# Kernel tuning notes

Measured on AMD Instinct MI355X. Metric: run time of the kernel, lower is better.

Reference implementation:

```python
import jax, jax.numpy as jnp
import numpy as np

D = 2048
N_HEADS = 16
N_KV = 4
HEAD_DIM = D // N_HEADS  # 128
N_REP = N_HEADS // N_KV  # 4
B, S = 2, 2048


def setup_inputs() -> dict:
    key = jax.random.key(0)
    ks = jax.random.split(key, 5)
    scale = 0.02
    return {
        "x": jax.random.normal(ks[0], (B, S, D), dtype=jnp.float32),
        "wq": jax.random.normal(ks[1], (D, N_HEADS * HEAD_DIM), dtype=jnp.float32) * scale,
        "wk": jax.random.normal(ks[2], (D, N_KV * HEAD_DIM), dtype=jnp.float32) * scale,
        "wv": jax.random.normal(ks[3], (D, N_KV * HEAD_DIM), dtype=jnp.float32) * scale,
        "wo": jax.random.normal(ks[4], (N_HEADS * HEAD_DIM, D), dtype=jnp.float32) * scale,
    }


def reference(x, wq, wk, wv, wo):
    b, s, _ = x.shape
    # projections
    xq = (x @ wq).reshape(b, s, N_HEADS, HEAD_DIM)
    xk = (x @ wk).reshape(b, s, N_KV, HEAD_DIM)
    xv = (x @ wv).reshape(b, s, N_KV, HEAD_DIM)
    # GQA: group queries per kv head -> [b, n_kv, n_rep, s, d]
    xq = xq.transpose(0, 2, 1, 3).reshape(b, N_KV, N_REP, s, HEAD_DIM)
    xk = xk.transpose(0, 2, 1, 3)  # [b, n_kv, s, d]
    xv = xv.transpose(0, 2, 1, 3)
    scale = 1.0 / jnp.sqrt(jnp.asarray(HEAD_DIM, dtype=x.dtype))
    scores = jnp.einsum('bkrqd,bkvd->bkrqv', xq, xk) * scale  # [b,n_kv,n_rep,s,s]
    causal = jnp.triu(jnp.ones((s, s), dtype=bool), k=1)
    scores = jnp.where(causal, jnp.asarray(-jnp.inf, dtype=scores.dtype), scores)
    probs = jax.nn.softmax(scores, axis=-1)
    out = jnp.einsum('bkrqv,bkvd->bkrqd', probs, xv)  # [b,n_kv,n_rep,s,d]
    out = out.reshape(b, N_HEADS, s, HEAD_DIM).transpose(0, 2, 1, 3).reshape(b, s, N_HEADS * HEAD_DIM)
    return out @ wo
```

## Files before the change

kernel.cpp:

```cpp
#include <hip/hip_runtime.h>

typedef unsigned short u16;
using bf16x8 = __attribute__((ext_vector_type(8))) short;
using f32x4  = __attribute__((ext_vector_type(4))) float;

#define ATTN_NEG (-3.0e38f)

__device__ __forceinline__ u16 f2bf_rne(float f) {
  unsigned int u = __float_as_uint(f);
  u += 0x7fffu + ((u >> 16) & 1u);
  return (u16)(u >> 16);
}

__device__ __forceinline__ void load_lds16(const u16* g, u16* l) {
  using gp = const __attribute__((address_space(1))) unsigned int*;
  using lp = __attribute__((address_space(3))) unsigned int*;
  __builtin_amdgcn_global_load_lds((gp)g, (lp)l, 16, 0, 0);
}

__device__ __forceinline__ void transpose_body(const float* __restrict__ in,
                                               u16* __restrict__ out, int K, int N,
                                               int bx, int by, int tid) {
  __shared__ float tile[32][33];
  int tx = tid & 31, ty = tid >> 5;
  int x0 = bx * 32, y0 = by * 32;
  #pragma unroll
  for (int i = 0; i < 32; i += 8)
    tile[ty + i][tx] = in[(size_t)(y0 + ty + i) * N + x0 + tx];
  __syncthreads();
  #pragma unroll
  for (int i = 0; i < 32; i += 8)
    out[(size_t)(x0 + ty + i) * K + y0 + tx] = f2bf_rne(tile[tx][ty + i]);
}

__global__ __launch_bounds__(256) void prep_kernel(const float* __restrict__ x,
                                                   const float* __restrict__ wq,
                                                   const float* __restrict__ wk,
                                                   const float* __restrict__ wv,
                                                   const float* __restrict__ wo,
                                                   u16* xb, u16* wqt, u16* wkt, u16* wvt,
                                                   u16* wot) {
  int bid = blockIdx.x, tid = threadIdx.x;
  if (bid < 8192) {
    int i = bid * 1024 + tid * 4;
    float4 v = *(const float4*)(x + i);
    u16* p = xb + i;
    p[0] = f2bf_rne(v.x); p[1] = f2bf_rne(v.y); p[2] = f2bf_rne(v.z); p[3] = f2bf_rne(v.w);
  } else if (bid < 12288) {
    int t = bid - 8192;
    transpose_body(wq, wqt, 2048, 2048, t & 63, t >> 6, tid);
  } else if (bid < 13312) {
    int t = bid - 12288;
    transpose_body(wk, wkt, 2048, 512, t & 15, t >> 4, tid);
  } else if (bid < 14336) {
    int t = bid - 13312;
    transpose_body(wv, wvt, 2048, 512, t & 15, t >> 4, tid);
  } else {
    int t = bid - 14336;
    transpose_body(wo, wot, 2048, 2048, t & 63, t >> 6, tid);
  }
}

template <int MODE>
__device__ __forceinline__ void gemm_tile(const u16* __restrict__ A, const u16* __restrict__ Bt,
                                          void* __restrict__ Cv, int M, int N, int K,
                                          int bx, int by, char* smem) {
  u16* As = (u16*)smem;
  u16* Bs = (u16*)(smem + 16384);
  const int tid  = threadIdx.x;
  const int wave = tid >> 6, lane = tid & 63;
  const int quad = lane >> 4, l16 = lane & 15;
  const int m0 = by * 128, n0 = bx * 128;
  const int wm = (wave >> 1) * 64, wn = (wave & 1) * 64;
  f32x4 acc[4][4] = {};

  const int srow = lane >> 2;
  const int scol = (lane & 3) << 3;

  for (int k0 = 0; k0 < K; k0 += 64) {
    __syncthreads();
    #pragma unroll
    for (int h = 0; h < 2; ++h)
      #pragma unroll
      for (int i = 0; i < 2; ++i) {
        const int row = wave * 16 + i * 64;
        load_lds16(A  + (size_t)(m0 + row + srow) * K + k0 + h * 32 + scol,
                   As + h * 4096 + row * 32);
        load_lds16(Bt + (size_t)(n0 + row + srow) * K + k0 + h * 32 + scol,
                   Bs + h * 4096 + row * 32);
      }
    __syncthreads();
    #pragma unroll
    for (int h = 0; h < 2; ++h) {
      bf16x8 af[4], bfr[4];
      #pragma unroll
      for (int i = 0; i < 4; ++i) {
        af[i]  = *(const bf16x8*)(As + h * 4096 + (wm + i * 16 + l16) * 32 + quad * 8);
        bfr[i] = *(const bf16x8*)(Bs + h * 4096 + (wn + i * 16 + l16) * 32 + quad * 8);
      }
      #pragma unroll
      for (int mi = 0; mi < 4; ++mi)
        #pragma unroll
        for (int ni = 0; ni < 4; ++ni)
          acc[mi][ni] =
              __builtin_amdgcn_mfma_f32_16x16x32_bf16(af[mi], bfr[ni], acc[mi][ni], 0, 0, 0);
    }
  }

  if constexpr (MODE == 0 || MODE == 3) {
    const float sc = (MODE == 3) ? 0.12751742f : 1.0f;
    u16* Cb = (u16*)Cv;
    #pragma unroll
    for (int mi = 0; mi < 4; ++mi)
      #pragma unroll
      for (int ni = 0; ni < 4; ++ni) {
        int row = m0 + wm + mi * 16 + quad * 4;
        int col = n0 + wn + ni * 16 + l16;
        #pragma unroll
        for (int r = 0; r < 4; ++r)
          Cb[(size_t)(row + r) * N + col] = f2bf_rne(acc[mi][ni][r] * sc);
      }
  } else if constexpr (MODE == 1) {
    u16* Cb = (u16*)Cv;
    #pragma unroll
    for (int mi = 0; mi < 4; ++mi)
      #pragma unroll
      for (int ni = 0; ni < 4; ++ni) {
        int col = n0 + wn + ni * 16 + l16;
        #pragma unroll
        for (int r = 0; r < 4; ++r) {
          int row = m0 + wm + mi * 16 + quad * 4 + r;
          int bb = row >> 11, s = row & 2047;
          int c = s & 31;
          int cp = ((c & 15) >> 2) * 8 + ((c >> 4) & 1) * 4 + (c & 3);
          Cb[((size_t)(bb * 512 + col)) * 2048 + (s & ~31) + cp] = f2bf_rne(acc[mi][ni][r]);
        }
      }
  } else {
    float* Cf = (float*)Cv;
    #pragma unroll
    for (int mi = 0; mi < 4; ++mi)
      #pragma unroll
      for (int ni = 0; ni < 4; ++ni) {
        int row = m0 + wm + mi * 16 + quad * 4;
        int col = n0 + wn + ni * 16 + l16;
        #pragma unroll
        for (int r = 0; r < 4; ++r)
          Cf[(size_t)(row + r) * N + col] = acc[mi][ni][r];
      }
  }
}

__global__ __launch_bounds__(256) void qkv_gemm(const u16* xb, const u16* wqt, const u16* wkt,
                                                const u16* wvt, u16* Qb, u16* Kb, u16* Vt) {
  extern __shared__ char smem[];
  int bx = blockIdx.x, by = blockIdx.y;
  if (bx < 16)
    gemm_tile<3>(xb, wqt, Qb, 4096, 2048, 2048, bx, by, smem);
  else if (bx < 20)
    gemm_tile<0>(xb, wkt, Kb, 4096, 512, 2048, bx - 16, by, smem);
  else
    gemm_tile<1>(xb, wvt, Vt, 4096, 512, 2048, bx - 20, by, smem);
}

template <int MODE>
__global__ __launch_bounds__(256) void gemm_kernel(const u16* A, const u16* Bt, void* C,
                                                   int M, int N, int K) {
  extern __shared__ char smem[];
  gemm_tile<MODE>(A, Bt, C, M, N, K, blockIdx.x, blockIdx.y, smem);
}


__device__ __forceinline__ void stage_kv64(const u16* __restrict__ Kg, const u16* __restrict__ Vg,
                                           int kt0, u16* __restrict__ kbuf,
                                           u16* __restrict__ vbuf,
                                           int wave, int quad, int l16) {
  #pragma unroll
  for (int c = 0; c < 2; ++c) {
    #pragma unroll
    for (int h = 0; h < 2; ++h)
      load_lds16(Kg + (size_t)(kt0 + 32 * c + h * 16 + l16) * 512 + wave * 32 + quad * 8,
                 kbuf + c * 4096 + (wave * 2 + h) * 512);
    #pragma unroll
    for (int i = 0; i < 2; ++i) {
      int f = wave * 2 + i;
      load_lds16(Vg + (size_t)(16 * f + l16) * 2048 + kt0 + 32 * c + quad * 8,
                 vbuf + c * 4096 + f * 512);
    }
  }
}

template <bool MASKED>
__device__ __forceinline__ void attn_compute64(const u16* __restrict__ kbuf,
                                               const u16* __restrict__ vbuf,
                                               int kt0, int q0w, int quad, int l16,
                                               const bf16x8 (&qf)[4], f32x4 (&o)[8],
                                               float& l_lane) {
  const int slot = (quad * 16 + l16) * 8;
  #pragma unroll
  for (int c = 0; c < 2; ++c) {
    const int kb = kt0 + 32 * c;
    if (MASKED && kb > q0w + 15) break;

    bf16x8 kf[8];
    #pragma unroll
    for (int kk = 0; kk < 8; ++kk)
      kf[kk] = *(const bf16x8*)(kbuf + c * 4096 + kk * 512 + slot);

    f32x4 sa[2] = {};
    __builtin_amdgcn_s_setprio(1);
    #pragma unroll
    for (int h = 0; h < 2; ++h)
      #pragma unroll
      for (int ks = 0; ks < 4; ++ks)
        sa[h] = __builtin_amdgcn_mfma_f32_16x16x32_bf16(kf[ks * 2 + h], qf[ks], sa[h], 0, 0, 0);
    __builtin_amdgcn_s_setprio(0);

    bf16x8 pc;
    #pragma unroll
    for (int h = 0; h < 2; ++h)
      #pragma unroll
      for (int r = 0; r < 4; ++r) {
        float s = sa[h][r];
        if (MASKED) {
          int kpos = kb + 16 * h + quad * 4 + r;
          s = (kpos <= q0w + l16) ? s : ATTN_NEG;
        }
        float p = __builtin_amdgcn_exp2f(s);
        l_lane += p;
        pc[h * 4 + r] = (short)f2bf_rne(p);
      }

    __builtin_amdgcn_s_setprio(1);
    #pragma unroll
    for (int f = 0; f < 8; ++f) {
      bf16x8 v8 = *(const bf16x8*)(vbuf + c * 4096 + f * 512 + slot);
      o[f] = __builtin_amdgcn_mfma_f32_16x16x32_bf16(pc, v8, o[f], 0, 0, 0);
    }
    __builtin_amdgcn_s_setprio(0);
  }
}

__global__ __launch_bounds__(256, 2) void attn_kernel(const u16* __restrict__ Qb,
                                                      const u16* __restrict__ Kb,
                                                      const u16* __restrict__ Vt,
                                                      u16* __restrict__ Ob) {
  constexpr int S = 2048;
  const int b = blockIdx.z, h = blockIdx.y, g = h >> 2, tp = blockIdx.x;
  const int tid = threadIdx.x;
  const int wave = tid >> 6, lane = tid & 63, quad = lane >> 4, l16 = lane & 15;
  __shared__ alignas(16) u16 Kt[2][8192];
  __shared__ alignas(16) u16 Vl[2][8192];
  __shared__ float lbuf[4][16];

  const u16* Kg = Kb + (size_t)b * S * 512 + g * 128;
  const u16* Vg = Vt + (size_t)(b * 512 + g * 128) * 2048;

  #pragma unroll
  for (int half = 0; half < 2; ++half) {
    const int tile = (half == 0) ? tp : 31 - tp;
    const int wrow = (half == 0) ? wave : 3 - wave;
    const int q0w = tile * 64 + wrow * 16;
    const int nsteps = tile + 1;

    bf16x8 qf[4];
    const u16* qrow = Qb + (size_t)(b * S + q0w + l16) * 2048 + h * 128 + quad * 8;
    #pragma unroll
    for (int ks = 0; ks < 4; ++ks) qf[ks] = *(const bf16x8*)(qrow + ks * 32);

    f32x4 o[8] = {};
    float l_lane = 0.f;

    __syncthreads();
    stage_kv64(Kg, Vg, 0, Kt[0], Vl[0], wave, quad, l16);

    for (int s = 0; s < nsteps; ++s) {
      __syncthreads();
      if (s + 1 < nsteps)
        stage_kv64(Kg, Vg, (s + 1) * 64, Kt[(s + 1) & 1], Vl[(s + 1) & 1], wave, quad, l16);
      if (s + 1 < nsteps)
        attn_compute64<false>(Kt[s & 1], Vl[s & 1], s * 64, q0w, quad, l16, qf, o, l_lane);
      else
        attn_compute64<true>(Kt[s & 1], Vl[s & 1], s * 64, q0w, quad, l16, qf, o, l_lane);
    }

    float lt = l_lane + __shfl_xor(l_lane, 16);
    lt += __shfl_xor(lt, 32);
    if (quad == 0) lbuf[wave][l16] = lt;
    __builtin_amdgcn_wave_barrier();
    float il[4];
    #pragma unroll
    for (int r = 0; r < 4; ++r) il[r] = 1.f / lbuf[wave][quad * 4 + r];

    u16* orow = Ob + (size_t)(b * S + q0w + quad * 4) * 2048 + h * 128 + l16;
    #pragma unroll
    for (int f = 0; f < 8; ++f)
      #pragma unroll
      for (int r = 0; r < 4; ++r)
        orow[(size_t)r * 2048 + f * 16] = f2bf_rne(o[f][r] * il[r]);
  }
}

extern "C" void kernel_launch(void* const* d_in, const int* in_sizes, int n_in,
                              void* d_out, int out_size, void* d_ws, size_t ws_size,
                              hipStream_t stream) {
  const float* x  = (const float*)d_in[0];
  const float* wq = (const float*)d_in[1];
  const float* wk = (const float*)d_in[2];
  const float* wv = (const float*)d_in[3];
  const float* wo = (const float*)d_in[4];
  float* out = (float*)d_out;
  char* ws = (char*)d_ws;

  u16* xb  = (u16*)(ws);
  u16* wqt = (u16*)(ws + 16777216);
  u16* wkt = (u16*)(ws + 25165824);
  u16* wvt = (u16*)(ws + 27262976);
  u16* wot = (u16*)(ws + 29360128);
  u16* Qb  = (u16*)(ws + 37748736);
  u16* Kb  = (u16*)(ws + 54525952);
  u16* Vt  = (u16*)(ws + 58720256);
  u16* Ab  = (u16*)(ws + 62914560);

  prep_kernel<<<18432, 256, 0, stream>>>(x, wq, wk, wv, wo, xb, wqt, wkt, wvt, wot);
  qkv_gemm<<<dim3(24, 32), 256, 32768, stream>>>(xb, wqt, wkt, wvt, Qb, Kb, Vt);
  attn_kernel<<<dim3(16, 16, 2), 256, 0, stream>>>(Qb, Kb, Vt, Ab);
  gemm_kernel<2><<<dim3(16, 32), 256, 32768, stream>>>(Ab, wot, out, 4096, 2048, 2048);
}
```

Measured before the change: 304.1 us.

## Load V tiles directly into registers with double-buffered prefetch instead of LDS

V fragments for each 64-key step are now fetched from global memory straight into per-lane registers (two ping-pong register sets), and the shared-memory V buffer is removed. The loop is manually unrolled by two with a partial vmcnt wait so that only the older loads must finish, overlapping the next step's K and V fetch with the current compute. This removes LDS writes, reads and capacity for V but adds 32 extra 128-bit registers per lane, which risks spilling or reduced occupancy under launch_bounds(256,2). It also always issues a redundant prefetch on the final step, and relies on a hand-counted vmcnt value being correct.

```diff
diff --git a/kernel.cpp b/kernel.cpp
--- a/kernel.cpp
+++ b/kernel.cpp
@@ -171,28 +171,28 @@
 }
 
 
-__device__ __forceinline__ void stage_kv64(const u16* __restrict__ Kg, const u16* __restrict__ Vg,
-                                           int kt0, u16* __restrict__ kbuf,
-                                           u16* __restrict__ vbuf,
-                                           int wave, int quad, int l16) {
-  #pragma unroll
-  for (int c = 0; c < 2; ++c) {
+__device__ __forceinline__ void stage_k64(const u16* __restrict__ Kg, int kt0,
+                                          u16* __restrict__ kbuf, int wave, int quad, int l16) {
+  #pragma unroll
+  for (int c = 0; c < 2; ++c)
     #pragma unroll
     for (int h = 0; h < 2; ++h)
       load_lds16(Kg + (size_t)(kt0 + 32 * c + h * 16 + l16) * 512 + wave * 32 + quad * 8,
                  kbuf + c * 4096 + (wave * 2 + h) * 512);
-    #pragma unroll
-    for (int i = 0; i < 2; ++i) {
-      int f = wave * 2 + i;
-      load_lds16(Vg + (size_t)(16 * f + l16) * 2048 + kt0 + 32 * c + quad * 8,
-                 vbuf + c * 4096 + f * 512);
-    }
-  }
+}
+
+__device__ __forceinline__ void load_v64(const u16* __restrict__ Vg, int kt0,
+                                         int quad, int l16, bf16x8 (&vv)[16]) {
+  #pragma unroll
+  for (int c = 0; c < 2; ++c)
+    #pragma unroll
+    for (int f = 0; f < 8; ++f)
+      vv[c * 8 + f] = *(const bf16x8*)(Vg + (size_t)(16 * f + l16) * 2048 + kt0 + 32 * c + quad * 8);
 }
 
 template <bool MASKED>
 __device__ __forceinline__ void attn_compute64(const u16* __restrict__ kbuf,
-                                               const u16* __restrict__ vbuf,
+                                               const bf16x8 (&vv)[16],
                                                int kt0, int q0w, int quad, int l16,
                                                const bf16x8 (&qf)[4], f32x4 (&o)[8],
                                                float& l_lane) {
@@ -233,13 +233,25 @@
 
     __builtin_amdgcn_s_setprio(1);
     #pragma unroll
-    for (int f = 0; f < 8; ++f) {
-      bf16x8 v8 = *(const bf16x8*)(vbuf + c * 4096 + f * 512 + slot);
-      o[f] = __builtin_amdgcn_mfma_f32_16x16x32_bf16(pc, v8, o[f], 0, 0, 0);
-    }
+    for (int f = 0; f < 8; ++f)
+      o[f] = __builtin_amdgcn_mfma_f32_16x16x32_bf16(pc, vv[c * 8 + f], o[f], 0, 0, 0);
     __builtin_amdgcn_s_setprio(0);
   }
 }
+
+#define ATTN_STEP(VVC, VVN)                                                          \
+  {                                                                                  \
+    asm volatile("s_waitcnt vmcnt(16)" ::: "memory");           \
+    __builtin_amdgcn_s_barrier();                             \
+    const int sn = (s + 1 < nsteps) ? s + 1 : s;           \
+    stage_k64(Kg, sn * 64, Kt[(s + 1) & 1], wave, quad, l16);                        \
+    __builtin_amdgcn_sched_barrier(0);                     \
+    load_v64(Vg, sn * 64, quad, l16, VVN);                                           \
+    if (s + 1 < nsteps)                                                              \
+      attn_compute64<false>(Kt[s & 1], VVC, s * 64, q0w, quad, l16, qf, o, l_lane);  \
+    else                                                                             \
+      attn_compute64<true>(Kt[s & 1], VVC, s * 64, q0w, quad, l16, qf, o, l_lane);   \
+  }
 
 __global__ __launch_bounds__(256, 2) void attn_kernel(const u16* __restrict__ Qb,
                                                       const u16* __restrict__ Kb,
@@ -250,7 +262,6 @@
   const int tid = threadIdx.x;
   const int wave = tid >> 6, lane = tid & 63, quad = lane >> 4, l16 = lane & 15;
   __shared__ alignas(16) u16 Kt[2][8192];
-  __shared__ alignas(16) u16 Vl[2][8192];
   __shared__ float lbuf[4][16];
 
   const u16* Kg = Kb + (size_t)b * S * 512 + g * 128;
@@ -270,18 +281,19 @@
 
     f32x4 o[8] = {};
     float l_lane = 0.f;
+    bf16x8 vvA[16], vvB[16];
 
     __syncthreads();
-    stage_kv64(Kg, Vg, 0, Kt[0], Vl[0], wave, quad, l16);
-
-    for (int s = 0; s < nsteps; ++s) {
-      __syncthreads();
-      if (s + 1 < nsteps)
-        stage_kv64(Kg, Vg, (s + 1) * 64, Kt[(s + 1) & 1], Vl[(s + 1) & 1], wave, quad, l16);
-      if (s + 1 < nsteps)
-        attn_compute64<false>(Kt[s & 1], Vl[s & 1], s * 64, q0w, quad, l16, qf, o, l_lane);
-      else
-        attn_compute64<true>(Kt[s & 1], Vl[s & 1], s * 64, q0w, quad, l16, qf, o, l_lane);
+    stage_k64(Kg, 0, Kt[0], wave, quad, l16);
+    __builtin_amdgcn_sched_barrier(0);
+    load_v64(Vg, 0, quad, l16, vvA);
+
+    for (int s = 0; s < nsteps;) {
+      ATTN_STEP(vvA, vvB);
+      ++s;
+      if (s == nsteps) break;
+      ATTN_STEP(vvB, vvA);
+      ++s;
     }
 
     float lt = l_lane + __shfl_xor(l_lane, 16);
```

Measured after the change: 573.9 us. 1.89x slower.
